# Optimization experiments

Measured on AMD Instinct MI355X. Metric: run time of the kernel, lower is better.

## Reference

```python
import jax, jax.numpy as jnp
import numpy as np

HEAD_DIM = 64
FEAT_H, FEAT_W = 64, 64
ROPE_THETA = 10000.0


def axial_rope_cache(dim, height, width, theta):
    # Matches compute_axial_rope_cache: interleaved cos/sin of shape [H*W, dim]
    theta_dim = (dim // 2) // 2
    freqs = 1.0 / theta ** (jnp.arange(theta_dim, dtype=jnp.float32) * 2.0 / theta_dim)
    t_x = jnp.tile(jnp.arange(width, dtype=jnp.float32)[None, :], (height, 1)).reshape(-1)
    t_y = jnp.tile(jnp.arange(height, dtype=jnp.float32)[:, None], (1, width)).reshape(-1)
    theta_all = jnp.concatenate([jnp.outer(t_x, freqs), jnp.outer(t_y, freqs)], axis=-1)
    cos = jnp.repeat(jnp.cos(theta_all), 2, axis=-1)  # [H*W, dim]
    sin = jnp.repeat(jnp.sin(theta_all), 2, axis=-1)
    return cos, sin


def apply_rope(x, cos, sin):
    # x: [B, H, N, D]; cos/sin: [N, D]
    x1 = x[..., 0::2]
    x2 = x[..., 1::2]
    rot = jnp.stack([-x2, x1], axis=-1).reshape(x.shape)
    return x * cos[None, None] + rot * sin[None, None]


def setup_inputs() -> dict:
    key = jax.random.key(0)
    ks = jax.random.split(key, 11)
    B, Nq, Nk, E, KVD, ID = 1, 4096, 8192, 256, 64, 256
    s_e = 1.0 / np.sqrt(E)
    s_kv = 1.0 / np.sqrt(KVD)
    s_i = 1.0 / np.sqrt(ID)
    return {
        "query": jax.random.normal(ks[0], (B, Nq, E), jnp.float32),
        "key": jax.random.normal(ks[1], (B, Nk, KVD), jnp.float32),
        "value": jax.random.normal(ks[2], (B, Nk, KVD), jnp.float32),
        "Wq": jax.random.normal(ks[3], (E, ID), jnp.float32) * s_e,
        "bq": jnp.zeros((ID,), jnp.float32),
        "Wk": jax.random.normal(ks[4], (KVD, ID), jnp.float32) * s_kv,
        "bk": jnp.zeros((ID,), jnp.float32),
        "Wv": jax.random.normal(ks[5], (KVD, ID), jnp.float32) * s_kv,
        "bv": jnp.zeros((ID,), jnp.float32),
        "Wo": jax.random.normal(ks[6], (ID, E), jnp.float32) * s_i,
        "bo": jnp.zeros((E,), jnp.float32),
        "num_k_exclude_rope": 0,
    }


def reference(query, key, value, Wq, bq, Wk, bk, Wv, bv, Wo, bo, num_k_exclude_rope):
    B, Nq, _ = query.shape
    Nk = key.shape[1]
    H, D = 4, HEAD_DIM

    def split_heads(x):
        b, n, c = x.shape
        return x.reshape(b, n, H, c // H).transpose(0, 2, 1, 3)

    q = split_heads(query @ Wq + bq)  # [B,H,Nq,D]
    k = split_heads(key @ Wk + bk)    # [B,H,Nk,D]
    v = split_heads(value @ Wv + bv)

    cos, sin = axial_rope_cache(D, FEAT_H, FEAT_W, ROPE_THETA)  # [4096, D]
    q = apply_rope(q, cos, sin)

    num_k_rope = Nk - num_k_exclude_rope
    k_spatial = k[:, :, :num_k_rope, :]
    k_other = k[:, :, num_k_rope:, :]
    repeats = num_k_rope // cos.shape[0]  # rope_k_repeat=True
    cos_k = jnp.tile(cos, (repeats, 1))
    sin_k = jnp.tile(sin, (repeats, 1))
    k_spatial = apply_rope(k_spatial, cos_k, sin_k)
    k = jnp.concatenate([k_spatial, k_other], axis=2)

    q = q / jnp.sqrt(jnp.asarray(D, q.dtype))
    scores = jnp.einsum("bhqd,bhkd->bhqk", q, k)
    attn = jax.nn.softmax(scores, axis=-1)
    out = jnp.einsum("bhqk,bhkd->bhqd", attn, v)
    out = out.transpose(0, 2, 1, 3).reshape(B, Nq, H * D)
    return out @ Wo + bo
```

## Files before the change

### kernel.cpp

```cpp
#include <hip/hip_runtime.h>
#include <hip/hip_bf16.h>

#define NQ 4096
#define NK 8192
#define NSPLIT 8
#define KSPAN (NK / NSPLIT)
#define BK 64

#define QSCALE 0.1803368801111204f

typedef short v8s __attribute__((ext_vector_type(8)));
typedef float v4f __attribute__((ext_vector_type(4)));

static __device__ __forceinline__ unsigned short f2bf(float f) {
    unsigned int u = __float_as_uint(f);
    u = (u + 0x7FFFu + ((u >> 16) & 1u)) >> 16;
    return (unsigned short)u;
}
static __device__ __forceinline__ float bf2f(unsigned short h) {
    return __uint_as_float(((unsigned int)h) << 16);
}
static __device__ __forceinline__ unsigned int pkbf(float a, float b) {
    union { __hip_bfloat162 h; unsigned int u; } cv;
    cv.h = __float22bfloat162_rn(make_float2(a, b));
    return cv.u;
}
static __device__ __forceinline__ void split8(const float* a, v8s& hi, v8s& lo) {
#pragma unroll
    for (int j = 0; j < 8; ++j) {
        unsigned short h = f2bf(a[j]);
        hi[j] = (short)h;
        lo[j] = (short)f2bf(a[j] - bf2f(h));
    }
}
static __device__ __forceinline__ void wload(const unsigned short* __restrict__ H,
                                             const unsigned short* __restrict__ L,
                                             int k0, int col, v8s& wh, v8s& wl) {
    const size_t f = (size_t)((k0 >> 3) * 256 + col) * 8;
    wh = *(const v8s*)(H + f);
    wl = *(const v8s*)(L + f);
}
static __device__ __forceinline__ void dma16(const unsigned short* g, unsigned short* l) {
    __builtin_amdgcn_global_load_lds(
        (const __attribute__((address_space(1))) unsigned int*)(const void*)g,
        (__attribute__((address_space(3))) unsigned int*)(void*)l, 16, 0, 0);
}

__global__ __launch_bounds__(256) void prep_kernel(
    const float* __restrict__ Wq, const float* __restrict__ Wk,
    const float* __restrict__ Wv, const float* __restrict__ Wo,
    unsigned short* __restrict__ WqH, unsigned short* __restrict__ WqL,
    unsigned short* __restrict__ WkH, unsigned short* __restrict__ WkL,
    unsigned short* __restrict__ WvH, unsigned short* __restrict__ WvL,
    unsigned short* __restrict__ WoH, unsigned short* __restrict__ WoL)
{
    const int tid = blockIdx.x * 256 + threadIdx.x;
    const float* W;
    unsigned short *H, *L;
    int f;
    if (tid < 8192)        { W = Wq; H = WqH; L = WqL; f = tid; }
    else if (tid < 10240)  { W = Wk; H = WkH; L = WkL; f = tid - 8192; }
    else if (tid < 12288)  { W = Wv; H = WvH; L = WvL; f = tid - 10240; }
    else                   { W = Wo; H = WoH; L = WoL; f = tid - 12288; }
    const int col = f & 255, k0 = (f >> 8) << 3;
    float wv[8];
#pragma unroll
    for (int j = 0; j < 8; ++j) wv[j] = W[(size_t)(k0 + j) * 256 + col];
    v8s hi, lo;
    split8(wv, hi, lo);
    *(v8s*)(H + (size_t)f * 8) = hi;
    *(v8s*)(L + (size_t)f * 8) = lo;
}

__global__ __launch_bounds__(256) void qkv_kernel(
    const float* __restrict__ query, const float* __restrict__ key,
    const float* __restrict__ value,
    const unsigned short* __restrict__ WqH, const unsigned short* __restrict__ WqL,
    const unsigned short* __restrict__ WkH, const unsigned short* __restrict__ WkL,
    const unsigned short* __restrict__ WvH, const unsigned short* __restrict__ WvL,
    const float* __restrict__ bq, const float* __restrict__ bk,
    const float* __restrict__ bv,
    unsigned short* __restrict__ Qb, unsigned short* __restrict__ Kb,
    unsigned short* __restrict__ Vt, const int* __restrict__ nexp)
{
    const int b = blockIdx.x;
    const int t = threadIdx.x, w = t >> 6, lane = t & 63;
    const int quad = lane >> 4, l16 = lane & 15;
    const int colbase = w * 64;

    if (b < 256) {
        const int n0 = b * 16;
        v4f acc[4];
#pragma unroll
        for (int ct = 0; ct < 4; ++ct) {
            const float bb = bq[colbase + ct * 16 + l16];
            acc[ct] = v4f{bb, bb, bb, bb};
        }
        const float* arow = query + (size_t)(n0 + l16) * 256 + quad * 8;
#pragma unroll
        for (int k0 = 0; k0 < 256; k0 += 32) {
            float av[8];
            *(float4*)av = *(const float4*)(arow + k0);
            *(float4*)(av + 4) = *(const float4*)(arow + k0 + 4);
            v8s ah, al;
            split8(av, ah, al);
#pragma unroll
            for (int ct = 0; ct < 4; ++ct) {
                v8s wh, wl;
                wload(WqH, WqL, k0 + quad * 8, colbase + ct * 16 + l16, wh, wl);
                acc[ct] = __builtin_amdgcn_mfma_f32_16x16x32_bf16(al, wh, acc[ct], 0, 0, 0);
                acc[ct] = __builtin_amdgcn_mfma_f32_16x16x32_bf16(ah, wl, acc[ct], 0, 0, 0);
                acc[ct] = __builtin_amdgcn_mfma_f32_16x16x32_bf16(ah, wh, acc[ct], 0, 0, 0);
            }
        }
#pragma unroll
        for (int ct = 0; ct < 4; ++ct) {
            const int d = ct * 16 + l16;
            const int j = d >> 1;
            const float freq = exp2f(-(float)(j & 15) * 1.66096404744368f);
            const bool isx = (j < 16), odd = (d & 1);
#pragma unroll
            for (int r = 0; r < 4; ++r) {
                const int p = n0 + quad * 4 + r;
                const float tpos = isx ? (float)(p & 63) : (float)(p >> 6);
                float sn, cs;
                __sincosf(tpos * freq, &sn, &cs);
                const float x = acc[ct][r];
                const float xp = __shfl_xor(x, 1, 64);
                const float y = odd ? fmaf(x, cs, xp * sn) : fmaf(x, cs, -xp * sn);
                Qb[((size_t)(w * NQ + p) << 6) + d] = f2bf(y * QSCALE);
            }
        }
    } else {
        const bool isK = (b < 768);
        const int n0 = (isK ? (b - 256) : (b - 768)) * 16;
        const float* X = isK ? key : value;
        const unsigned short* WH = isK ? WkH : WvH;
        const unsigned short* WL = isK ? WkL : WvL;
        const float* bias = isK ? bk : bv;
        v4f acc[4];
#pragma unroll
        for (int ct = 0; ct < 4; ++ct) {
            const float bb = bias[colbase + ct * 16 + l16];
            acc[ct] = v4f{bb, bb, bb, bb};
        }
        const float* arow = X + (size_t)(n0 + l16) * 64 + quad * 8;
#pragma unroll
        for (int k0 = 0; k0 < 64; k0 += 32) {
            float av[8];
            *(float4*)av = *(const float4*)(arow + k0);
            *(float4*)(av + 4) = *(const float4*)(arow + k0 + 4);
            v8s ah, al;
            split8(av, ah, al);
#pragma unroll
            for (int ct = 0; ct < 4; ++ct) {
                v8s wh, wl;
                wload(WH, WL, k0 + quad * 8, colbase + ct * 16 + l16, wh, wl);
                acc[ct] = __builtin_amdgcn_mfma_f32_16x16x32_bf16(al, wh, acc[ct], 0, 0, 0);
                acc[ct] = __builtin_amdgcn_mfma_f32_16x16x32_bf16(ah, wl, acc[ct], 0, 0, 0);
                acc[ct] = __builtin_amdgcn_mfma_f32_16x16x32_bf16(ah, wh, acc[ct], 0, 0, 0);
            }
        }
        if (isK) {
            const int nro = NK - *nexp;
#pragma unroll
            for (int ct = 0; ct < 4; ++ct) {
                const int d = ct * 16 + l16;
                const int j = d >> 1;
                const float freq = exp2f(-(float)(j & 15) * 1.66096404744368f);
                const bool isx = (j < 16), odd = (d & 1);
#pragma unroll
                for (int r = 0; r < 4; ++r) {
                    const int p = n0 + quad * 4 + r;
                    const int pc = p & 4095;
                    const float tpos = isx ? (float)(pc & 63) : (float)(pc >> 6);
                    float sn, cs;
                    __sincosf(tpos * freq, &sn, &cs);
                    const float x = acc[ct][r];
                    const float xp = __shfl_xor(x, 1, 64);
                    float y = odd ? fmaf(x, cs, xp * sn) : fmaf(x, cs, -xp * sn);
                    y = (p < nro) ? y : x;
                    Kb[((size_t)(w * NK + p) << 6) + d] = f2bf(y);
                }
            }
        } else {
#pragma unroll
            for (int ct = 0; ct < 4; ++ct) {
                const int col = colbase + ct * 16 + l16;
                uint2 u = make_uint2(pkbf(acc[ct][0], acc[ct][1]),
                                     pkbf(acc[ct][2], acc[ct][3]));
                *(uint2*)(Vt + (size_t)col * NK + n0 + quad * 4) = u;
            }
        }
    }
}

__global__ __launch_bounds__(256) void attn_kernel(
    const unsigned short* __restrict__ Qb, const unsigned short* __restrict__ Kb,
    const unsigned short* __restrict__ Vt, unsigned short* __restrict__ Opart,
    float* __restrict__ Lbuf)
{
    __shared__ alignas(16) unsigned short Kl[2][64 * 64];
    __shared__ alignas(16) unsigned short Vl[2][64 * 64];

    const int blk = blockIdx.x;
    const int s = blk & 7, h = (blk >> 3) & 3, qt = blk >> 5;
    const int t = threadIdx.x;
    const int w = t >> 6, lane = t & 63;
    const int quad = lane >> 4, l16 = lane & 15;

    const int q0 = qt * 128 + w * 32;
    v8s qf[2][2];
#pragma unroll
    for (int g = 0; g < 2; ++g) {
        const unsigned short* qr = Qb + ((size_t)(h * NQ + q0 + g * 16 + l16) << 6) + quad * 8;
        qf[g][0] = *(const v8s*)qr;
        qf[g][1] = *(const v8s*)(qr + 32);
    }

    v4f O[4][2];
#pragma unroll
    for (int dt = 0; dt < 4; ++dt)
#pragma unroll
        for (int g = 0; g < 2; ++g) O[dt][g] = v4f{0.f, 0.f, 0.f, 0.f};
    float psum[2] = {0.f, 0.f};

    const unsigned short* Kbase = Kb + (((size_t)h * NK + s * KSPAN) << 6);
    const unsigned short* Vbase = Vt + (size_t)(h * 64) * NK + s * KSPAN;

    const int srow = lane >> 3;
    const int schunk = (lane & 7) ^ srow;
    const int c0off = ((quad ^ (l16 & 7)) * 8);
    const int c1off = c0off ^ 32;
    int voff[2][2];
#pragma unroll
    for (int tv = 0; tv < 2; ++tv)
#pragma unroll
        for (int h2 = 0; h2 < 2; ++h2)
            voff[tv][h2] = (((4 * tv + 2 * h2 + (quad >> 1)) ^ (l16 & 7)) << 3) + 4 * (quad & 1);

    const int NT = KSPAN / BK;

#pragma unroll
    for (int half = 0; half < 2; ++half) {
        const int r0 = w * 16 + half * 8;
        dma16(Kbase + ((size_t)(r0 + srow) << 6) + schunk * 8, &Kl[0][r0 * 64]);
        dma16(Vbase + (size_t)(r0 + srow) * NK + schunk * 8, &Vl[0][r0 * 64]);
    }

    for (int it = 0; it < NT; ++it) {
        const int cur = it & 1;
        __syncthreads();

        if (it + 1 < NT) {
            const int k1 = (it + 1) * BK;
#pragma unroll
            for (int half = 0; half < 2; ++half) {
                const int r0 = w * 16 + half * 8;
                dma16(Kbase + ((size_t)(k1 + r0 + srow) << 6) + schunk * 8, &Kl[cur ^ 1][r0 * 64]);
                dma16(Vbase + (size_t)(r0 + srow) * NK + k1 + schunk * 8, &Vl[cur ^ 1][r0 * 64]);
            }
        }

        const unsigned short* Klc = &Kl[cur][0];
        const unsigned short* Vlc = &Vl[cur][0];

        v8s pf[2][2];
#pragma unroll
        for (int tt = 0; tt < 4; ++tt) {
            const unsigned short* kr = &Klc[(tt * 16 + l16) * 64];
            const v8s kf0 = *(const v8s*)(kr + c0off);
            const v8s kf1 = *(const v8s*)(kr + c1off);
#pragma unroll
            for (int g = 0; g < 2; ++g) {
                v4f a = v4f{0.f, 0.f, 0.f, 0.f};
                a = __builtin_amdgcn_mfma_f32_16x16x32_bf16(kf0, qf[g][0], a, 0, 0, 0);
                a = __builtin_amdgcn_mfma_f32_16x16x32_bf16(kf1, qf[g][1], a, 0, 0, 0);
                const float e0 = __builtin_amdgcn_exp2f(a[0]);
                const float e1 = __builtin_amdgcn_exp2f(a[1]);
                const float e2 = __builtin_amdgcn_exp2f(a[2]);
                const float e3 = __builtin_amdgcn_exp2f(a[3]);
                psum[g] += (e0 + e1) + (e2 + e3);
                unsigned int* pp = (unsigned int*)&pf[g][tt >> 1];
                pp[(tt & 1) * 2 + 0] = pkbf(e0, e1);
                pp[(tt & 1) * 2 + 1] = pkbf(e2, e3);
            }
        }

#pragma unroll
        for (int dt = 0; dt < 4; ++dt) {
            const unsigned short* vr = &Vlc[(dt * 16 + l16) * 64];
#pragma unroll
            for (int tv = 0; tv < 2; ++tv) {
                union { v8s s; uint2 u[2]; } vv;
                vv.u[0] = *(const uint2*)(vr + voff[tv][0]);
                vv.u[1] = *(const uint2*)(vr + voff[tv][1]);
#pragma unroll
                for (int g = 0; g < 2; ++g)
                    O[dt][g] = __builtin_amdgcn_mfma_f32_16x16x32_bf16(vv.s, pf[g][tv], O[dt][g], 0, 0, 0);
            }
        }
    }

#pragma unroll
    for (int g = 0; g < 2; ++g) {
        float p = psum[g];
        p += __shfl_xor(p, 16, 64);
        p += __shfl_xor(p, 32, 64);
        psum[g] = p;
    }
    unsigned short* Ob = Opart + (size_t)blk * 8192;
#pragma unroll
    for (int g = 0; g < 2; ++g) {
        const int row = w * 32 + g * 16 + l16;
#pragma unroll
        for (int dt = 0; dt < 4; ++dt) {
            uint2 u = make_uint2(pkbf(O[dt][g][0], O[dt][g][1]),
                                 pkbf(O[dt][g][2], O[dt][g][3]));
            *(uint2*)(Ob + row * 64 + dt * 16 + quad * 4) = u;
        }
        if (quad == 0) Lbuf[blk * 128 + row] = psum[g];
    }
}

__global__ __launch_bounds__(256) void oreduce_kernel(
    const unsigned short* __restrict__ Opart, const float* __restrict__ Lbuf,
    unsigned short* __restrict__ OredH, unsigned short* __restrict__ OredL)
{
    const int tid = blockIdx.x * 256 + threadIdx.x;
    const int e0 = tid << 3;
    const int r = e0 >> 8, d0 = e0 & 255;
    const int h = d0 >> 6;
    const int qt = r >> 7, rr = r & 127;
    const int base = qt * 32 + h * 8;
    const unsigned short* op = Opart + (size_t)base * 8192 + rr * 64 + (d0 & 63);
    float lsum = 0.f;
    float o[8] = {0.f, 0.f, 0.f, 0.f, 0.f, 0.f, 0.f, 0.f};
#pragma unroll
    for (int s = 0; s < NSPLIT; ++s) {
        lsum += Lbuf[(base + s) * 128 + rr];
        v8s a = *(const v8s*)(op + (size_t)s * 8192);
#pragma unroll
        for (int j = 0; j < 8; ++j) o[j] += bf2f((unsigned short)a[j]);
    }
    const float inv = 1.f / lsum;
#pragma unroll
    for (int j = 0; j < 8; ++j) o[j] *= inv;
    v8s hi, lo;
    split8(o, hi, lo);
    *(v8s*)(OredH + (size_t)r * 256 + d0) = hi;
    *(v8s*)(OredL + (size_t)r * 256 + d0) = lo;
}

__global__ __launch_bounds__(256) void oproj_kernel(
    const unsigned short* __restrict__ OredH, const unsigned short* __restrict__ OredL,
    const unsigned short* __restrict__ WoH, const unsigned short* __restrict__ WoL,
    const float* __restrict__ bo, float* __restrict__ out)
{
    const int t = threadIdx.x, w = t >> 6, lane = t & 63;
    const int quad = lane >> 4, l16 = lane & 15;
    const int n0 = (blockIdx.x >> 2) * 16;
    const int col = (blockIdx.x & 3) * 64 + w * 16 + l16;
    const float bb = bo[col];
    v4f acc = v4f{bb, bb, bb, bb};
    const unsigned short* ah_row = OredH + (size_t)(n0 + l16) * 256 + quad * 8;
    const unsigned short* al_row = OredL + (size_t)(n0 + l16) * 256 + quad * 8;
#pragma unroll
    for (int k0 = 0; k0 < 256; k0 += 32) {
        v8s ah = *(const v8s*)(ah_row + k0);
        v8s al = *(const v8s*)(al_row + k0);
        v8s wh, wl;
        wload(WoH, WoL, k0 + quad * 8, col, wh, wl);
        acc = __builtin_amdgcn_mfma_f32_16x16x32_bf16(al, wh, acc, 0, 0, 0);
        acc = __builtin_amdgcn_mfma_f32_16x16x32_bf16(ah, wl, acc, 0, 0, 0);
        acc = __builtin_amdgcn_mfma_f32_16x16x32_bf16(ah, wh, acc, 0, 0, 0);
    }
#pragma unroll
    for (int r = 0; r < 4; ++r)
        out[(size_t)(n0 + quad * 4 + r) * 256 + col] = acc[r];
}

extern "C" void kernel_launch(void* const* d_in, const int* in_sizes, int n_in,
                              void* d_out, int out_size, void* d_ws, size_t ws_size,
                              hipStream_t stream) {
    const float* query = (const float*)d_in[0];
    const float* key   = (const float*)d_in[1];
    const float* value = (const float*)d_in[2];
    const float* Wq    = (const float*)d_in[3];
    const float* bq    = (const float*)d_in[4];
    const float* Wk    = (const float*)d_in[5];
    const float* bk    = (const float*)d_in[6];
    const float* Wv    = (const float*)d_in[7];
    const float* bv    = (const float*)d_in[8];
    const float* Wo    = (const float*)d_in[9];
    const float* bo    = (const float*)d_in[10];
    const int*   nex   = (const int*)d_in[11];

    char* ws = (char*)d_ws;
    const size_t MB = 1024 * 1024;
    unsigned short* Qb    = (unsigned short*)(ws);
    unsigned short* Kb    = (unsigned short*)(ws + 2 * MB);
    unsigned short* Vt    = (unsigned short*)(ws + 6 * MB);
    unsigned short* Opart = (unsigned short*)(ws + 10 * MB);
    float* Lbuf           = (float*)(ws + 26 * MB);
    unsigned short* OredH = (unsigned short*)(ws + 26 * MB + 512 * 1024);
    unsigned short* OredL = (unsigned short*)(ws + 28 * MB + 512 * 1024);
    unsigned short* Wpl   = (unsigned short*)(ws + 30 * MB + 512 * 1024);
    unsigned short* WqH = Wpl;
    unsigned short* WqL = Wpl + 65536;
    unsigned short* WkH = Wpl + 131072;
    unsigned short* WkL = Wpl + 147456;
    unsigned short* WvH = Wpl + 163840;
    unsigned short* WvL = Wpl + 180224;
    unsigned short* WoH = Wpl + 196608;
    unsigned short* WoL = Wpl + 262144;
    float* out = (float*)d_out;

    prep_kernel<<<80, 256, 0, stream>>>(Wq, Wk, Wv, Wo,
                                        WqH, WqL, WkH, WkL, WvH, WvL, WoH, WoL);
    qkv_kernel<<<1280, 256, 0, stream>>>(query, key, value,
                                         WqH, WqL, WkH, WkL, WvH, WvL,
                                         bq, bk, bv, Qb, Kb, Vt, nex);
    attn_kernel<<<1024, 256, 0, stream>>>(Qb, Kb, Vt, Opart, Lbuf);
    oreduce_kernel<<<512, 256, 0, stream>>>(Opart, Lbuf, OredH, OredL);
    oproj_kernel<<<256 * 4, 256, 0, stream>>>(OredH, OredL, WoH, WoL, bo, out);
}
```

Measured before the change: 160.2 us.

## Double attention K-splits and fuse split reduction into output projection

Raises the number of key splits in the attention kernel from 8 to 16, doubling the grid to 2048 blocks so more work is in flight per CU. The separate reduction kernel is folded into the output projection kernel, which sums the partials and normalizes them into LDS before running the MFMA projection. This removes one launch and the round trip of the reduced hi/lo buffers through global memory. In exchange, the partial-output buffer and the reduction reads double, and each attention block processes fewer key tiles to amortize its Q load and epilogue.

```diff
diff --git a/kernel.cpp b/kernel.cpp
--- a/kernel.cpp
+++ b/kernel.cpp
@@ -3,7 +3,7 @@
 
 #define NQ 4096
 #define NK 8192
-#define NSPLIT 8
+#define NSPLIT 16
 #define KSPAN (NK / NSPLIT)
 #define BK 64
 
@@ -204,7 +204,7 @@
     __shared__ alignas(16) unsigned short Vl[2][64 * 64];
 
     const int blk = blockIdx.x;
-    const int s = blk & 7, h = (blk >> 3) & 3, qt = blk >> 5;
+    const int s = blk & 15, h = (blk >> 4) & 3, qt = blk >> 6;
     const int t = threadIdx.x;
     const int w = t >> 6, lane = t & 63;
     const int quad = lane >> 4, l16 = lane & 15;
@@ -323,61 +323,72 @@
     }
 }
 
-__global__ __launch_bounds__(256) void oreduce_kernel(
+__global__ __launch_bounds__(512) void oproj_kernel(
     const unsigned short* __restrict__ Opart, const float* __restrict__ Lbuf,
-    unsigned short* __restrict__ OredH, unsigned short* __restrict__ OredL)
-{
-    const int tid = blockIdx.x * 256 + threadIdx.x;
-    const int e0 = tid << 3;
-    const int r = e0 >> 8, d0 = e0 & 255;
-    const int h = d0 >> 6;
-    const int qt = r >> 7, rr = r & 127;
-    const int base = qt * 32 + h * 8;
-    const unsigned short* op = Opart + (size_t)base * 8192 + rr * 64 + (d0 & 63);
-    float lsum = 0.f;
-    float o[8] = {0.f, 0.f, 0.f, 0.f, 0.f, 0.f, 0.f, 0.f};
-#pragma unroll
-    for (int s = 0; s < NSPLIT; ++s) {
-        lsum += Lbuf[(base + s) * 128 + rr];
-        v8s a = *(const v8s*)(op + (size_t)s * 8192);
-#pragma unroll
-        for (int j = 0; j < 8; ++j) o[j] += bf2f((unsigned short)a[j]);
-    }
-    const float inv = 1.f / lsum;
-#pragma unroll
-    for (int j = 0; j < 8; ++j) o[j] *= inv;
-    v8s hi, lo;
-    split8(o, hi, lo);
-    *(v8s*)(OredH + (size_t)r * 256 + d0) = hi;
-    *(v8s*)(OredL + (size_t)r * 256 + d0) = lo;
-}
-
-__global__ __launch_bounds__(256) void oproj_kernel(
-    const unsigned short* __restrict__ OredH, const unsigned short* __restrict__ OredL,
     const unsigned short* __restrict__ WoH, const unsigned short* __restrict__ WoL,
     const float* __restrict__ bo, float* __restrict__ out)
 {
-    const int t = threadIdx.x, w = t >> 6, lane = t & 63;
+    __shared__ alignas(16) unsigned short AH[16][264];
+    __shared__ alignas(16) unsigned short AL[16][264];
+
+    const int blk = blockIdx.x;
+    const int n0 = blk * 16;
+    const int qt = n0 >> 7, rr0 = n0 & 127;
+    const int t = threadIdx.x;
+
+    {
+        const int row = t >> 5;
+        const int d0 = (t & 31) * 8;
+        const int h = d0 >> 6, dd0 = d0 & 63;
+        const int rr = rr0 + row;
+        const int base = qt * 64 + h * 16;
+        const unsigned short* op = Opart + (size_t)base * 8192 + rr * 64 + dd0;
+        float lsum = 0.f;
+        float o[8] = {0.f, 0.f, 0.f, 0.f, 0.f, 0.f, 0.f, 0.f};
+#pragma unroll
+        for (int s = 0; s < NSPLIT; ++s) {
+            lsum += Lbuf[(base + s) * 128 + rr];
+            v8s a = *(const v8s*)(op + (size_t)s * 8192);
+#pragma unroll
+            for (int j = 0; j < 8; ++j) o[j] += bf2f((unsigned short)a[j]);
+        }
+        const float inv = 1.f / lsum;
+#pragma unroll
+        for (int j = 0; j < 8; ++j) o[j] *= inv;
+        v8s hi, lo;
+        split8(o, hi, lo);
+        *(v8s*)&AH[row][d0] = hi;
+        *(v8s*)&AL[row][d0] = lo;
+    }
+    __syncthreads();
+
+    const int w = t >> 6, lane = t & 63;
     const int quad = lane >> 4, l16 = lane & 15;
-    const int n0 = (blockIdx.x >> 2) * 16;
-    const int col = (blockIdx.x & 3) * 64 + w * 16 + l16;
-    const float bb = bo[col];
-    v4f acc = v4f{bb, bb, bb, bb};
-    const unsigned short* ah_row = OredH + (size_t)(n0 + l16) * 256 + quad * 8;
-    const unsigned short* al_row = OredL + (size_t)(n0 + l16) * 256 + quad * 8;
+    const int colbase = w * 32;
+    v4f acc[2];
+#pragma unroll
+    for (int ct = 0; ct < 2; ++ct) {
+        const float bb = bo[colbase + ct * 16 + l16];
+        acc[ct] = v4f{bb, bb, bb, bb};
+    }
 #pragma unroll
     for (int k0 = 0; k0 < 256; k0 += 32) {
-        v8s ah = *(const v8s*)(ah_row + k0);
-        v8s al = *(const v8s*)(al_row + k0);
-        v8s wh, wl;
-        wload(WoH, WoL, k0 + quad * 8, col, wh, wl);
-        acc = __builtin_amdgcn_mfma_f32_16x16x32_bf16(al, wh, acc, 0, 0, 0);
-        acc = __builtin_amdgcn_mfma_f32_16x16x32_bf16(ah, wl, acc, 0, 0, 0);
-        acc = __builtin_amdgcn_mfma_f32_16x16x32_bf16(ah, wh, acc, 0, 0, 0);
-    }
-#pragma unroll
-    for (int r = 0; r < 4; ++r)
-        out[(size_t)(n0 + quad * 4 + r) * 256 + col] = acc[r];
+        const v8s ah = *(const v8s*)&AH[l16][k0 + quad * 8];
+        const v8s al = *(const v8s*)&AL[l16][k0 + quad * 8];
+#pragma unroll
+        for (int ct = 0; ct < 2; ++ct) {
+            v8s wh, wl;
+            wload(WoH, WoL, k0 + quad * 8, colbase + ct * 16 + l16, wh, wl);
+            acc[ct] = __builtin_amdgcn_mfma_f32_16x16x32_bf16(al, wh, acc[ct], 0, 0, 0);
+            acc[ct] = __builtin_amdgcn_mfma_f32_16x16x32_bf16(ah, wl, acc[ct], 0, 0, 0);
+            acc[ct] = __builtin_amdgcn_mfma_f32_16x16x32_bf16(ah, wh, acc[ct], 0, 0, 0);
+        }
+    }
+#pragma unroll
+    for (int ct = 0; ct < 2; ++ct)
+#pragma unroll
+        for (int r = 0; r < 4; ++r)
+            out[(size_t)(n0 + quad * 4 + r) * 256 + colbase + ct * 16 + l16] = acc[ct][r];
 }
 
 extern "C" void kernel_launch(void* const* d_in, const int* in_sizes, int n_in,
@@ -402,10 +413,8 @@
     unsigned short* Kb    = (unsigned short*)(ws + 2 * MB);
     unsigned short* Vt    = (unsigned short*)(ws + 6 * MB);
     unsigned short* Opart = (unsigned short*)(ws + 10 * MB);
-    float* Lbuf           = (float*)(ws + 26 * MB);
-    unsigned short* OredH = (unsigned short*)(ws + 26 * MB + 512 * 1024);
-    unsigned short* OredL = (unsigned short*)(ws + 28 * MB + 512 * 1024);
-    unsigned short* Wpl   = (unsigned short*)(ws + 30 * MB + 512 * 1024);
+    float* Lbuf           = (float*)(ws + 42 * MB);
+    unsigned short* Wpl   = (unsigned short*)(ws + 43 * MB);
     unsigned short* WqH = Wpl;
     unsigned short* WqL = Wpl + 65536;
     unsigned short* WkH = Wpl + 131072;
@@ -421,7 +430,6 @@
     qkv_kernel<<<1280, 256, 0, stream>>>(query, key, value,
                                          WqH, WqL, WkH, WkL, WvH, WvL,
                                          bq, bk, bv, Qb, Kb, Vt, nex);
-    attn_kernel<<<1024, 256, 0, stream>>>(Qb, Kb, Vt, Opart, Lbuf);
-    oreduce_kernel<<<512, 256, 0, stream>>>(Opart, Lbuf, OredH, OredL);
-    oproj_kernel<<<256 * 4, 256, 0, stream>>>(OredH, OredL, WoH, WoL, bo, out);
-}
+    attn_kernel<<<2048, 256, 0, stream>>>(Qb, Kb, Vt, Opart, Lbuf);
+    oproj_kernel<<<256, 512, 0, stream>>>(Opart, Lbuf, WoH, WoL, bo, out);
+}
```

Result: faster. 155.2 us (-3.1%).
